# Kernel tuning notes

Hardware: AMD Instinct MI355X
Metric: run time of the kernel (lower is better)

The kernel has to match this reference:

```python
import jax, jax.numpy as jnp
import numpy as np

B = 2048
C = 32            # num_categories
STATE_DIM = 64    # state_input_dim
EMB = 256         # emb_dim
OUT = 256         # output_dim
OBS_DIM = 512


def _cat_linear(x, W_all, b_all, cat_ids):
    # x: [B,S,din]; W_all: [C,din,dout]; b_all: [C,dout]; cat_ids: [B]
    W = W_all[cat_ids]            # [B,din,dout]  (per-sample weight gather)
    b = b_all[cat_ids]            # [B,dout]
    return jnp.einsum('bsd,bdh->bsh', x, W) + b[:, None, :]


def setup_inputs() -> dict:
    key = jax.random.key(0)
    ks = jax.random.split(key, 8)
    state = jax.random.normal(ks[0], (B, STATE_DIM), dtype=jnp.float32)
    obs = jax.random.uniform(ks[1], (B, 1, OBS_DIM), dtype=jnp.float32)
    cat_ids = jax.random.randint(ks[2], (B,), 0, C)
    obs_W = 0.01 * jax.random.normal(ks[3], (OBS_DIM, EMB), dtype=jnp.float32)
    obs_b = jnp.zeros((EMB,), dtype=jnp.float32)
    state_W = 0.02 * jax.random.normal(ks[4], (C, STATE_DIM, EMB), dtype=jnp.float32)
    state_b = jnp.zeros((C, EMB), dtype=jnp.float32)
    l2_W = 0.02 * jax.random.normal(ks[5], (C, 2 * EMB, OUT), dtype=jnp.float32)
    l2_b = jnp.zeros((C, OUT), dtype=jnp.float32)
    return {"state": state, "obs": obs, "cat_ids": cat_ids,
            "obs_W": obs_W, "obs_b": obs_b,
            "state_W": state_W, "state_b": state_b,
            "l2_W": l2_W, "l2_b": l2_b}


def reference(state, obs, cat_ids, obs_W, obs_b, state_W, state_b, l2_W, l2_b):
    # ObsEncoder (modeled as a linear projection): [B,1,OBS_DIM] -> [B,1,EMB]
    obs_emb = jnp.einsum('bsd,dh->bsh', obs, obs_W) + obs_b
    # state: [B,STATE_DIM] -> [B,1,STATE_DIM]
    state3 = state[:, None, :]
    state_emb = jax.nn.relu(_cat_linear(state3, state_W, state_b, cat_ids))  # [B,1,EMB]
    x = jnp.concatenate((state_emb, obs_emb), axis=2)                        # [B,1,2*EMB]
    return _cat_linear(x, l2_W, l2_b, cat_ids)                               # [B,1,OUT]
```

## Files before the change

kernel.cpp:

```cpp
#include <hip/hip_runtime.h>

constexpr int B_N   = 2048;
constexpr int C_N   = 32;
constexpr int SD    = 64;
constexpr int EMB   = 256;
constexpr int OUTD  = 256;
constexpr int OBSD  = 512;
constexpr int XDIM  = 512;
constexpr int CAP   = 256;

typedef __attribute__((ext_vector_type(8))) short bf16x8;
typedef __attribute__((ext_vector_type(4))) short bf16x4;
typedef __attribute__((ext_vector_type(4))) float f32x4;

constexpr size_t OFF_ROWS  = 4096;
constexpr size_t OFF_POBS  = 65536;
constexpr size_t OFF_PSTAT = 327680;
constexpr size_t OFF_PL2   = 1376256;
constexpr size_t NEED_L2   = OFF_PL2 + (size_t)C_N * XDIM * OUTD * 2;

__device__ __forceinline__ unsigned short bf_cvt(float f) {
    union { float f; unsigned u; } x; x.f = f;
    unsigned r = x.u + 0x7FFF + ((x.u >> 16) & 1);
    return (unsigned short)(r >> 16);
}

__global__ __launch_bounds__(256) void prep_kernel(
    const int* __restrict__ cat_ids,
    const float* __restrict__ obs_W, const float* __restrict__ state_W,
    const float* __restrict__ l2_W,
    int* __restrict__ counts, int* __restrict__ rows,
    unsigned short* __restrict__ p_obs, unsigned short* __restrict__ p_state,
    unsigned short* __restrict__ p_l2, int do_l2) {
    const int bid = blockIdx.x;
    const int t = threadIdx.x;

    if (bid < C_N) {
        __shared__ int cnt;
        __shared__ int list[CAP];
        if (t == 0) cnt = 0;
        __syncthreads();
        const int c = bid;
        for (int r = t; r < B_N; r += 256) {
            if (cat_ids[r] == c) {
                int s = atomicAdd(&cnt, 1);
                if (s < CAP) list[s] = r;
            }
        }
        __syncthreads();
        int n = min(cnt, CAP);
        for (int s = t; s < n; s += 256) rows[c * CAP + s] = list[s];
        if (t == 0) counts[c] = n;
        return;
    }

    const float* src;
    unsigned short* dst;
    {
        int pb = bid - C_N;
        if (pb < 16) {
            src = obs_W + (size_t)pb * 32 * 256;
            dst = p_obs + (size_t)pb * 8192;
        } else if (pb < 80) {
            int i = pb - 16;
            int mat = i >> 1, ch = i & 1;
            src = state_W + ((size_t)mat * SD + ch * 32) * 256;
            dst = p_state + (size_t)i * 8192;
        } else {
            if (!do_l2) return;
            int i = pb - 80;
            int mat = i >> 4, ch = i & 15;
            src = l2_W + ((size_t)mat * XDIM + ch * 32) * 256;
            dst = p_l2 + (size_t)i * 8192;
        }
    }

    __shared__ __align__(16) unsigned short sW[32 * 264];
    #pragma unroll
    for (int i2 = 0; i2 < 8; ++i2) {
        int f = t + 256 * i2;
        int row = f >> 6, c4 = f & 63;
        float4 v = ((const float4*)src)[f];
        unsigned short* d = &sW[row * 264 + c4 * 4];
        d[0] = bf_cvt(v.x); d[1] = bf_cvt(v.y); d[2] = bf_cvt(v.z); d[3] = bf_cvt(v.w);
    }
    __syncthreads();
    #pragma unroll
    for (int s4 = 0; s4 < 4; ++s4) {
        int slot = s4 * 256 + t;
        int strip = slot >> 6, lane = slot & 63;
        int r0 = (lane >> 4) * 8, col = strip * 16 + (lane & 15);
        unsigned short v[8];
        #pragma unroll
        for (int j = 0; j < 8; ++j) v[j] = sW[(r0 + j) * 264 + col];
        *(bf16x8*)(dst + (size_t)slot * 8) = *(bf16x8*)v;
    }
}

__global__ __launch_bounds__(512) void fused_kernel(
    const float* __restrict__ state, const float* __restrict__ obs,
    const float* __restrict__ obs_b, const float* __restrict__ state_b,
    const float* __restrict__ l2_W, const float* __restrict__ l2_b,
    const int* __restrict__ counts, const int* __restrict__ rows,
    const unsigned short* __restrict__ p_obs,
    const unsigned short* __restrict__ p_state,
    const unsigned short* __restrict__ p_l2, int has_pl2,
    float* __restrict__ out) {
    const int c = blockIdx.x;
    const int tile = blockIdx.y;
    const int n = counts[c];
    const int rbase = tile * 16;
    if (rbase >= n) return;
    const int nr = min(16, n - rbase);

    __shared__ __align__(16) unsigned short sAs[16 * 72];
    __shared__ __align__(16) unsigned short sAo[16 * 520];
    __shared__ __align__(16) unsigned short sX[16 * 520];
    __shared__ int sRows[16];

    const int t = threadIdx.x;
    const int w = t >> 6, l = t & 63;
    const int ml = l & 15, quad = l >> 4;

    if (t < 16) sRows[t] = (t < nr) ? rows[c * CAP + rbase + t] : 0;

    const bf16x8* pb1 = (const bf16x8*)(p_state + (size_t)c * SD * 256);
    const bf16x8* pb2 = (const bf16x8*)p_obs;
    bf16x8 pf1[4], pf2[12];
    #pragma unroll
    for (int kk = 0; kk < 2; ++kk)
        #pragma unroll
        for (int si = 0; si < 2; ++si)
            pf1[kk * 2 + si] = pb1[(kk * 16 + w * 2 + si) * 64 + l];
    #pragma unroll
    for (int kk = 0; kk < 6; ++kk)
        #pragma unroll
        for (int si = 0; si < 2; ++si)
            pf2[kk * 2 + si] = pb2[(kk * 16 + w * 2 + si) * 64 + l];

    __syncthreads();

    if (t < 256) {
        int i = t >> 4, c4 = t & 15;
        unsigned short vv[4] = {0, 0, 0, 0};
        if (i < nr) {
            float4 v = ((const float4*)(state + (size_t)sRows[i] * SD))[c4];
            vv[0] = bf_cvt(v.x); vv[1] = bf_cvt(v.y); vv[2] = bf_cvt(v.z); vv[3] = bf_cvt(v.w);
        }
        *(bf16x4*)&sAs[i * 72 + c4 * 4] = *(bf16x4*)vv;
    }
    #pragma unroll
    for (int i2 = 0; i2 < 4; ++i2) {
        int f = t + 512 * i2;
        int i = f >> 7, c4 = f & 127;
        unsigned short vv[4] = {0, 0, 0, 0};
        if (i < nr) {
            float4 v = ((const float4*)(obs + (size_t)sRows[i] * OBSD))[c4];
            vv[0] = bf_cvt(v.x); vv[1] = bf_cvt(v.y); vv[2] = bf_cvt(v.z); vv[3] = bf_cvt(v.w);
        }
        *(bf16x4*)&sAo[i * 520 + c4 * 4] = *(bf16x4*)vv;
    }
    __syncthreads();

    {
        f32x4 acc[2];
        #pragma unroll
        for (int si = 0; si < 2; ++si) acc[si] = (f32x4){0.f, 0.f, 0.f, 0.f};
        #pragma unroll
        for (int kk = 0; kk < 2; ++kk) {
            bf16x8 a = *(const bf16x8*)&sAs[ml * 72 + kk * 32 + quad * 8];
            #pragma unroll
            for (int si = 0; si < 2; ++si)
                acc[si] = __builtin_amdgcn_mfma_f32_16x16x32_bf16(a, pf1[kk * 2 + si], acc[si], 0, 0, 0);
        }
        #pragma unroll
        for (int si = 0; si < 2; ++si) {
            int colb = (w * 2 + si) * 16 + ml;
            float bias = state_b[c * 256 + colb];
            #pragma unroll
            for (int r = 0; r < 4; ++r)
                sX[(quad * 4 + r) * 520 + colb] = bf_cvt(fmaxf(acc[si][r] + bias, 0.f));
        }
    }

    {
        f32x4 acc[2];
        #pragma unroll
        for (int si = 0; si < 2; ++si) acc[si] = (f32x4){0.f, 0.f, 0.f, 0.f};
        #pragma unroll
        for (int kk = 0; kk < 16; ++kk) {
            bf16x8 a = *(const bf16x8*)&sAo[ml * 520 + kk * 32 + quad * 8];
            #pragma unroll
            for (int si = 0; si < 2; ++si) {
                int slot = (kk % 6) * 2 + si;
                bf16x8 b = pf2[slot];
                if (kk < 10)
                    pf2[slot] = pb2[((kk + 6) * 16 + w * 2 + si) * 64 + l];
                acc[si] = __builtin_amdgcn_mfma_f32_16x16x32_bf16(a, b, acc[si], 0, 0, 0);
            }
        }
        #pragma unroll
        for (int si = 0; si < 2; ++si) {
            int colb = (w * 2 + si) * 16 + ml;
            float bias = obs_b[colb];
            #pragma unroll
            for (int r = 0; r < 4; ++r)
                sX[(quad * 4 + r) * 520 + 256 + colb] = bf_cvt(acc[si][r] + bias);
        }
    }

    const bf16x8* pb3 = (const bf16x8*)p_l2 + (size_t)c * 16384;
    bf16x8 pf3[12];
    if (has_pl2) {
        #pragma unroll
        for (int kk = 0; kk < 6; ++kk)
            #pragma unroll
            for (int si = 0; si < 2; ++si)
                pf3[kk * 2 + si] = pb3[(kk * 16 + w * 2 + si) * 64 + l];
    }
    __syncthreads();

    {
        f32x4 acc[2];
        #pragma unroll
        for (int si = 0; si < 2; ++si) acc[si] = (f32x4){0.f, 0.f, 0.f, 0.f};
        if (has_pl2) {
            #pragma unroll
            for (int kk = 0; kk < 16; ++kk) {
                bf16x8 a = *(const bf16x8*)&sX[ml * 520 + kk * 32 + quad * 8];
                #pragma unroll
                for (int si = 0; si < 2; ++si) {
                    int slot = (kk % 6) * 2 + si;
                    bf16x8 b = pf3[slot];
                    if (kk < 10)
                        pf3[slot] = pb3[((kk + 6) * 16 + w * 2 + si) * 64 + l];
                    acc[si] = __builtin_amdgcn_mfma_f32_16x16x32_bf16(a, b, acc[si], 0, 0, 0);
                }
            }
        } else {
            for (int kk = 0; kk < 16; ++kk) {
                bf16x8 a = *(const bf16x8*)&sX[ml * 520 + kk * 32 + quad * 8];
                #pragma unroll
                for (int si = 0; si < 2; ++si) {
                    const float* wsrc = l2_W + ((size_t)c * XDIM + kk * 32 + quad * 8) * 256
                                        + (w * 2 + si) * 16 + ml;
                    bf16x8 b;
                    #pragma unroll
                    for (int j = 0; j < 8; ++j) b[j] = (short)bf_cvt(wsrc[j * 256]);
                    acc[si] = __builtin_amdgcn_mfma_f32_16x16x32_bf16(a, b, acc[si], 0, 0, 0);
                }
            }
        }
        #pragma unroll
        for (int si = 0; si < 2; ++si) {
            int colb = (w * 2 + si) * 16 + ml;
            float bias = l2_b[c * 256 + colb];
            #pragma unroll
            for (int r = 0; r < 4; ++r) {
                int row = quad * 4 + r;
                if (row < nr)
                    out[(size_t)sRows[row] * 256 + colb] = acc[si][r] + bias;
            }
        }
    }
}

extern "C" void kernel_launch(void* const* d_in, const int* in_sizes, int n_in,
                              void* d_out, int out_size, void* d_ws, size_t ws_size,
                              hipStream_t stream) {
    const float* state   = (const float*)d_in[0];
    const float* obs     = (const float*)d_in[1];
    const int*   cat_ids = (const int*)d_in[2];
    const float* obs_W   = (const float*)d_in[3];
    const float* obs_b   = (const float*)d_in[4];
    const float* state_W = (const float*)d_in[5];
    const float* state_b = (const float*)d_in[6];
    const float* l2_W    = (const float*)d_in[7];
    const float* l2_b    = (const float*)d_in[8];
    float* out = (float*)d_out;

    char* ws = (char*)d_ws;
    int* counts  = (int*)ws;
    int* rowsbuf = (int*)(ws + OFF_ROWS);
    unsigned short* p_obs  = (unsigned short*)(ws + OFF_POBS);
    unsigned short* p_stat = (unsigned short*)(ws + OFF_PSTAT);
    unsigned short* p_l2   = (unsigned short*)(ws + OFF_PL2);
    const int do_l2 = (ws_size >= NEED_L2) ? 1 : 0;

    int prep_blocks = C_N + 16 + 64 + (do_l2 ? 512 : 0);
    prep_kernel<<<dim3(prep_blocks), dim3(256), 0, stream>>>(
        cat_ids, obs_W, state_W, l2_W, counts, rowsbuf, p_obs, p_stat, p_l2, do_l2);

    fused_kernel<<<dim3(C_N, CAP / 16), dim3(512), 0, stream>>>(
        state, obs, obs_b, state_b, l2_W, l2_b, counts, rowsbuf,
        p_obs, p_stat, p_l2, do_l2, out);
}
```

Baseline: 98.16 us.

## Process 32 rows per block to reuse weight fragments across two M-tiles

Each block now handles 32 rows of a category instead of 16, issuing two MFMA M-tiles per loaded weight fragment and halving the grid's y dimension. Each weight fragment is read once per 32 rows instead of once per 16, which cuts global weight traffic per row. The row-index staging now reads rows directly from global memory, removing the first barrier. In exchange the kernel uses more shared memory and accumulators, and with about 64 rows per category there are fewer blocks, so parallelism drops.

```diff
diff --git a/kernel.cpp b/kernel.cpp
--- a/kernel.cpp
+++ b/kernel.cpp
@@ -109,20 +109,19 @@
     const int c = blockIdx.x;
     const int tile = blockIdx.y;
     const int n = counts[c];
-    const int rbase = tile * 16;
+    const int rbase = tile * 32;
     if (rbase >= n) return;
-    const int nr = min(16, n - rbase);
-
-    __shared__ __align__(16) unsigned short sAs[16 * 72];
-    __shared__ __align__(16) unsigned short sAo[16 * 520];
-    __shared__ __align__(16) unsigned short sX[16 * 520];
-    __shared__ int sRows[16];
+    const int nr = min(32, n - rbase);
+
+    __shared__ __align__(16) unsigned short sAs[32 * 72];
+    __shared__ __align__(16) unsigned short sAo[32 * 520];
+    __shared__ __align__(16) unsigned short sX[32 * 520];
+    __shared__ int sRows[32];
 
     const int t = threadIdx.x;
     const int w = t >> 6, l = t & 63;
     const int ml = l & 15, quad = l >> 4;
-
-    if (t < 16) sRows[t] = (t < nr) ? rows[c * CAP + rbase + t] : 0;
+    const int* rowp = rows + c * CAP + rbase;
 
     const bf16x8* pb1 = (const bf16x8*)(p_state + (size_t)c * SD * 256);
     const bf16x8* pb2 = (const bf16x8*)p_obs;
@@ -138,24 +137,26 @@
         for (int si = 0; si < 2; ++si)
             pf2[kk * 2 + si] = pb2[(kk * 16 + w * 2 + si) * 64 + l];
 
-    __syncthreads();
-
-    if (t < 256) {
+    if (t < 32) sRows[t] = (t < nr) ? rowp[t] : 0;
+
+    {
         int i = t >> 4, c4 = t & 15;
         unsigned short vv[4] = {0, 0, 0, 0};
         if (i < nr) {
-            float4 v = ((const float4*)(state + (size_t)sRows[i] * SD))[c4];
+            int ridx = rowp[i];
+            float4 v = ((const float4*)(state + (size_t)ridx * SD))[c4];
             vv[0] = bf_cvt(v.x); vv[1] = bf_cvt(v.y); vv[2] = bf_cvt(v.z); vv[3] = bf_cvt(v.w);
         }
         *(bf16x4*)&sAs[i * 72 + c4 * 4] = *(bf16x4*)vv;
     }
     #pragma unroll
-    for (int i2 = 0; i2 < 4; ++i2) {
+    for (int i2 = 0; i2 < 8; ++i2) {
         int f = t + 512 * i2;
         int i = f >> 7, c4 = f & 127;
         unsigned short vv[4] = {0, 0, 0, 0};
         if (i < nr) {
-            float4 v = ((const float4*)(obs + (size_t)sRows[i] * OBSD))[c4];
+            int ridx = rowp[i];
+            float4 v = ((const float4*)(obs + (size_t)ridx * OBSD))[c4];
             vv[0] = bf_cvt(v.x); vv[1] = bf_cvt(v.y); vv[2] = bf_cvt(v.z); vv[3] = bf_cvt(v.w);
         }
         *(bf16x4*)&sAo[i * 520 + c4 * 4] = *(bf16x4*)vv;
@@ -163,40 +164,51 @@
     __syncthreads();
 
     {
-        f32x4 acc[2];
-        #pragma unroll
-        for (int si = 0; si < 2; ++si) acc[si] = (f32x4){0.f, 0.f, 0.f, 0.f};
+        f32x4 acc[2][2];
+        #pragma unroll
+        for (int mt = 0; mt < 2; ++mt)
+            #pragma unroll
+            for (int si = 0; si < 2; ++si) acc[mt][si] = (f32x4){0.f, 0.f, 0.f, 0.f};
         #pragma unroll
         for (int kk = 0; kk < 2; ++kk) {
-            bf16x8 a = *(const bf16x8*)&sAs[ml * 72 + kk * 32 + quad * 8];
-            #pragma unroll
-            for (int si = 0; si < 2; ++si)
-                acc[si] = __builtin_amdgcn_mfma_f32_16x16x32_bf16(a, pf1[kk * 2 + si], acc[si], 0, 0, 0);
+            #pragma unroll
+            for (int mt = 0; mt < 2; ++mt) {
+                bf16x8 a = *(const bf16x8*)&sAs[(mt * 16 + ml) * 72 + kk * 32 + quad * 8];
+                #pragma unroll
+                for (int si = 0; si < 2; ++si)
+                    acc[mt][si] = __builtin_amdgcn_mfma_f32_16x16x32_bf16(a, pf1[kk * 2 + si], acc[mt][si], 0, 0, 0);
+            }
         }
         #pragma unroll
         for (int si = 0; si < 2; ++si) {
             int colb = (w * 2 + si) * 16 + ml;
             float bias = state_b[c * 256 + colb];
             #pragma unroll
-            for (int r = 0; r < 4; ++r)
-                sX[(quad * 4 + r) * 520 + colb] = bf_cvt(fmaxf(acc[si][r] + bias, 0.f));
-        }
-    }
-
-    {
-        f32x4 acc[2];
-        #pragma unroll
-        for (int si = 0; si < 2; ++si) acc[si] = (f32x4){0.f, 0.f, 0.f, 0.f};
+            for (int mt = 0; mt < 2; ++mt)
+                #pragma unroll
+                for (int r = 0; r < 4; ++r)
+                    sX[(mt * 16 + quad * 4 + r) * 520 + colb] = bf_cvt(fmaxf(acc[mt][si][r] + bias, 0.f));
+        }
+    }
+
+    {
+        f32x4 acc[2][2];
+        #pragma unroll
+        for (int mt = 0; mt < 2; ++mt)
+            #pragma unroll
+            for (int si = 0; si < 2; ++si) acc[mt][si] = (f32x4){0.f, 0.f, 0.f, 0.f};
         #pragma unroll
         for (int kk = 0; kk < 16; ++kk) {
-            bf16x8 a = *(const bf16x8*)&sAo[ml * 520 + kk * 32 + quad * 8];
+            bf16x8 a0 = *(const bf16x8*)&sAo[ml * 520 + kk * 32 + quad * 8];
+            bf16x8 a1 = *(const bf16x8*)&sAo[(16 + ml) * 520 + kk * 32 + quad * 8];
             #pragma unroll
             for (int si = 0; si < 2; ++si) {
                 int slot = (kk % 6) * 2 + si;
                 bf16x8 b = pf2[slot];
                 if (kk < 10)
                     pf2[slot] = pb2[((kk + 6) * 16 + w * 2 + si) * 64 + l];
-                acc[si] = __builtin_amdgcn_mfma_f32_16x16x32_bf16(a, b, acc[si], 0, 0, 0);
+                acc[0][si] = __builtin_amdgcn_mfma_f32_16x16x32_bf16(a0, b, acc[0][si], 0, 0, 0);
+                acc[1][si] = __builtin_amdgcn_mfma_f32_16x16x32_bf16(a1, b, acc[1][si], 0, 0, 0);
             }
         }
         #pragma unroll
@@ -204,8 +216,10 @@
             int colb = (w * 2 + si) * 16 + ml;
             float bias = obs_b[colb];
             #pragma unroll
-            for (int r = 0; r < 4; ++r)
-                sX[(quad * 4 + r) * 520 + 256 + colb] = bf_cvt(acc[si][r] + bias);
+            for (int mt = 0; mt < 2; ++mt)
+                #pragma unroll
+                for (int r = 0; r < 4; ++r)
+                    sX[(mt * 16 + quad * 4 + r) * 520 + 256 + colb] = bf_cvt(acc[mt][si][r] + bias);
         }
     }
 
@@ -221,25 +235,30 @@
     __syncthreads();
 
     {
-        f32x4 acc[2];
-        #pragma unroll
-        for (int si = 0; si < 2; ++si) acc[si] = (f32x4){0.f, 0.f, 0.f, 0.f};
+        f32x4 acc[2][2];
+        #pragma unroll
+        for (int mt = 0; mt < 2; ++mt)
+            #pragma unroll
+            for (int si = 0; si < 2; ++si) acc[mt][si] = (f32x4){0.f, 0.f, 0.f, 0.f};
         if (has_pl2) {
             #pragma unroll
             for (int kk = 0; kk < 16; ++kk) {
-                bf16x8 a = *(const bf16x8*)&sX[ml * 520 + kk * 32 + quad * 8];
+                bf16x8 a0 = *(const bf16x8*)&sX[ml * 520 + kk * 32 + quad * 8];
+                bf16x8 a1 = *(const bf16x8*)&sX[(16 + ml) * 520 + kk * 32 + quad * 8];
                 #pragma unroll
                 for (int si = 0; si < 2; ++si) {
                     int slot = (kk % 6) * 2 + si;
                     bf16x8 b = pf3[slot];
                     if (kk < 10)
                         pf3[slot] = pb3[((kk + 6) * 16 + w * 2 + si) * 64 + l];
-                    acc[si] = __builtin_amdgcn_mfma_f32_16x16x32_bf16(a, b, acc[si], 0, 0, 0);
+                    acc[0][si] = __builtin_amdgcn_mfma_f32_16x16x32_bf16(a0, b, acc[0][si], 0, 0, 0);
+                    acc[1][si] = __builtin_amdgcn_mfma_f32_16x16x32_bf16(a1, b, acc[1][si], 0, 0, 0);
                 }
             }
         } else {
             for (int kk = 0; kk < 16; ++kk) {
-                bf16x8 a = *(const bf16x8*)&sX[ml * 520 + kk * 32 + quad * 8];
+                bf16x8 a0 = *(const bf16x8*)&sX[ml * 520 + kk * 32 + quad * 8];
+                bf16x8 a1 = *(const bf16x8*)&sX[(16 + ml) * 520 + kk * 32 + quad * 8];
                 #pragma unroll
                 for (int si = 0; si < 2; ++si) {
                     const float* wsrc = l2_W + ((size_t)c * XDIM + kk * 32 + quad * 8) * 256
@@ -247,7 +266,8 @@
                     bf16x8 b;
                     #pragma unroll
                     for (int j = 0; j < 8; ++j) b[j] = (short)bf_cvt(wsrc[j * 256]);
-                    acc[si] = __builtin_amdgcn_mfma_f32_16x16x32_bf16(a, b, acc[si], 0, 0, 0);
+                    acc[0][si] = __builtin_amdgcn_mfma_f32_16x16x32_bf16(a0, b, acc[0][si], 0, 0, 0);
+                    acc[1][si] = __builtin_amdgcn_mfma_f32_16x16x32_bf16(a1, b, acc[1][si], 0, 0, 0);
                 }
             }
         }
@@ -256,11 +276,13 @@
             int colb = (w * 2 + si) * 16 + ml;
             float bias = l2_b[c * 256 + colb];
             #pragma unroll
-            for (int r = 0; r < 4; ++r) {
-                int row = quad * 4 + r;
-                if (row < nr)
-                    out[(size_t)sRows[row] * 256 + colb] = acc[si][r] + bias;
-            }
+            for (int mt = 0; mt < 2; ++mt)
+                #pragma unroll
+                for (int r = 0; r < 4; ++r) {
+                    int row = mt * 16 + quad * 4 + r;
+                    if (row < nr)
+                        out[(size_t)sRows[row] * 256 + colb] = acc[mt][si][r] + bias;
+                }
         }
     }
 }
@@ -291,7 +313,7 @@
     prep_kernel<<<dim3(prep_blocks), dim3(256), 0, stream>>>(
         cat_ids, obs_W, state_W, l2_W, counts, rowsbuf, p_obs, p_stat, p_l2, do_l2);
 
-    fused_kernel<<<dim3(C_N, CAP / 16), dim3(512), 0, stream>>>(
+    fused_kernel<<<dim3(C_N, CAP / 32), dim3(512), 0, stream>>>(
         state, obs, obs_b, state_b, l2_W, l2_b, counts, rowsbuf,
         p_obs, p_stat, p_l2, do_l2, out);
 }
```

Measured after the change: 104.2 us. +6.2%, slower.
